# Kernel optimization log

Measured on AMD Instinct MI355X. Metric: run time of the kernel, lower is better.

The kernel has to match this reference:

```python
import jax, jax.numpy as jnp
import numpy as np

B, S, C, D, K = 8, 1024, 8192, 256, 512
FREEDOM = 0.1

def setup_inputs() -> dict:
    key = jax.random.key(0)
    k1, k2, k3 = jax.random.split(key, 3)
    concept_seq = jax.random.uniform(k1, (B, S, C), dtype=jnp.float32)
    concept_emb = jax.random.uniform(k2, (C, D), dtype=jnp.float32)  # nn.Parameter(torch.rand(max_c+1, d_model))
    centroid_emb = jax.random.uniform(k3, (K, D), dtype=jnp.float32)
    return {"concept_seq": concept_seq, "concept_emb": concept_emb,
            "centroid_emb": centroid_emb, "domain": 0}

def reference(concept_seq, concept_emb, centroid_emb, domain):
    # normalize multi-hot rows by their count (rows summing to 0 use count=1)
    cnt = jnp.sum(concept_seq, axis=-1, keepdims=True)
    cnt = jnp.where(cnt == 0, jnp.ones_like(cnt), cnt)
    cs = concept_seq / cnt
    # weighted embedding sum: [B,S,C] @ [C,D] -> [B,S,D]
    e_free = jnp.einsum('bsc,cd->bsd', cs, concept_emb)
    # nearest centroid (argmin of cdist == argmin of squared distance)
    flat = e_free.reshape(-1, D)                               # [B*S, D]
    d2 = (jnp.sum(flat * flat, axis=1, keepdims=True)
          - 2.0 * flat @ centroid_emb.T
          + jnp.sum(centroid_emb * centroid_emb, axis=1))      # [B*S, K]
    idx = jnp.argmin(d2, axis=1)                               # [B*S]
    e_cent = centroid_emb[idx].reshape(e_free.shape)           # [B,S,D]
    return e_free * FREEDOM + e_cent * (1.0 - FREEDOM)
```

## Files before the change

### kernel.cpp

```cpp
#include <hip/hip_runtime.h>


typedef unsigned short u16;
typedef unsigned int   u32;
using bf16x8 = __attribute__((ext_vector_type(8))) short;
using f32x4  = __attribute__((ext_vector_type(4))) float;
using f32x16 = __attribute__((ext_vector_type(16))) float;

#define MFMA_B16(A,B,C) __builtin_amdgcn_mfma_f32_16x16x32_bf16((A),(B),(C),0,0,0)
#define MFMA32(A,B,C)   __builtin_amdgcn_mfma_f32_32x32x16_bf16((A),(B),(C),0,0,0)

#define NSPLIT 4
#define SWZ(r) ((((r)&7) ^ (((r)>>3)&3)))

static __device__ __forceinline__ u16 f2bf(float f){
  u32 u = __builtin_bit_cast(u32, f);
  u += 0x7FFFu + ((u >> 16) & 1u);
  return (u16)(u >> 16);
}
static __device__ __forceinline__ u16 f2bf_fast(float f){
  u32 u = __builtin_bit_cast(u32, f);
  return (u16)((u + 0x8000u) >> 16);
}
static __device__ __forceinline__ float bf2f(u16 h){
  u32 u = ((u32)h) << 16;
  return __builtin_bit_cast(float, u);
}
static __device__ __forceinline__ void split2(float va, float vb, u32& hw, u32& lw){
  u16 ha = f2bf(va), hb = f2bf(vb);
  hw = (u32)ha | ((u32)hb << 16);
  lw = (u32)f2bf(va - bf2f(ha)) | ((u32)f2bf(vb - bf2f(hb)) << 16);
}
static __device__ __forceinline__ void split2f(float va, float vb, u32& hw, u32& lw){
  u16 ha = f2bf_fast(va), hb = f2bf_fast(vb);
  hw = (u32)ha | ((u32)hb << 16);
  lw = (u32)f2bf_fast(va - bf2f(ha)) | ((u32)f2bf_fast(vb - bf2f(hb)) << 16);
}

#define SZ_PART    ((size_t)NSPLIT*8192UL*256UL*4UL)
#define OFF_CNT    (SZ_PART)
#define SZ_CNT     ((size_t)NSPLIT*8192UL*4UL)
#define OFF_BHI    (OFF_CNT + SZ_CNT)
#define SZ_BHI     (8192UL*256UL*2UL)
#define OFF_BLO    (OFF_BHI + SZ_BHI)
#define OFF_CTHI   (OFF_BLO + SZ_BHI)
#define SZ_CT      (512UL*256UL*2UL)
#define OFF_CTLO   (OFF_CTHI + SZ_CT)
#define OFF_CNORM  (OFF_CTLO + SZ_CT)

__global__ __launch_bounds__(256) void ce_prep(
    const float* __restrict__ emb, const float* __restrict__ cent,
    u16* __restrict__ Bhi, u16* __restrict__ Blo,
    u16* __restrict__ CThi, u16* __restrict__ CTlo,
    double* __restrict__ cnormd)
{
  const int b = blockIdx.x, t = threadIdx.x;
  const int l = t & 63;
  if (b < 1024) {
    const int g  = b * 4 + (t >> 6);
    const int nt = g >> 9, ksg = g & 511;
    const int col = nt*32 + (l & 31);
    const int k0  = ksg*16 + (l >> 5)*8;
    u32 hw[4], lw[4];
    #pragma unroll
    for (int p = 0; p < 4; ++p) {
      float va = emb[(size_t)(k0 + 2*p    )*256 + col];
      float vb = emb[(size_t)(k0 + 2*p + 1)*256 + col];
      split2(va, vb, hw[p], lw[p]);
    }
    const size_t fi = ((size_t)nt*512 + ksg)*64 + l;
    *(uint4*)(Bhi + fi*8) = make_uint4(hw[0],hw[1],hw[2],hw[3]);
    *(uint4*)(Blo + fi*8) = make_uint4(lw[0],lw[1],lw[2],lw[3]);
  } else if (b < 1088) {
    const int lr = l & 15, lk = l >> 4;
    const int g  = (b - 1024) * 4 + (t >> 6);
    const int nt = g >> 3, ksg = g & 7;
    u32 hw[4], lw[4];
    #pragma unroll
    for (int p = 0; p < 4; ++p) {
      float va = cent[(size_t)(nt*16 + lr)*256 + ksg*32 + lk*8 + 2*p    ] - 0.5f;
      float vb = cent[(size_t)(nt*16 + lr)*256 + ksg*32 + lk*8 + 2*p + 1] - 0.5f;
      split2(va, vb, hw[p], lw[p]);
    }
    const size_t fi = ((size_t)nt*8 + ksg)*64 + l;
    *(uint4*)(CThi + fi*8) = make_uint4(hw[0],hw[1],hw[2],hw[3]);
    *(uint4*)(CTlo + fi*8) = make_uint4(lw[0],lw[1],lw[2],lw[3]);
  } else {
    const int row = (b - 1088)*8 + (t >> 5);
    const int h = t & 31;
    double s = 0.0;
    #pragma unroll
    for (int j = 0; j < 8; ++j) {
      float x = cent[(size_t)row*256 + h*8 + j] - 0.5f;
      s += (double)x * (double)x;
    }
    #pragma unroll
    for (int off = 16; off > 0; off >>= 1) s += __shfl_xor(s, off);
    if (h == 0) cnormd[row] = s;
  }
}

__global__ __launch_bounds__(512, 4) void ce_gemm(
    const float* __restrict__ seq,
    const u16* __restrict__ Bhi, const u16* __restrict__ Blo,
    float* __restrict__ part, float* __restrict__ cntpart)
{
  __shared__ char Ah[2][2*64*128];
  __shared__ char Al[2][2*64*128];

  const int t   = threadIdx.x;
  const int blk = blockIdx.x;
  const int mt  = blk >> 2;
  const int ks  = blk & 3;
  const size_t rowBase = (size_t)mt * 64;
  const int ar  = t >> 3;
  const int ac  = t & 7;
  const float* aptr = seq + (rowBase + ar) * 8192 + (size_t)ks * 2048 + ac * 16;

  const int w = t >> 6, l = t & 63;
  const int lrow = l & 31, lhi = l >> 5;

  f32x16 acc0 = {0.f}, acc1 = {0.f};
  #pragma unroll
  for (int i = 0; i < 16; ++i) { acc0[i] = 0.f; acc1[i] = 0.f; }

  float csum = 0.f;
  float4 areg[4];

  auto loadA = [&](void) {
    #pragma unroll
    for (int i = 0; i < 4; ++i) areg[i] = *(const float4*)(aptr + i*4);
  };
  auto stage8 = [&](int buf, int j) {
    const float4 A = areg[2*j], B = areg[2*j+1];
    float v[8] = {A.x, A.y, A.z, A.w, B.x, B.y, B.z, B.w};
    #pragma unroll
    for (int i = 0; i < 8; ++i) csum += v[i];
    u32 hw[4], lw[4];
    #pragma unroll
    for (int p = 0; p < 4; ++p) split2f(v[2*p], v[2*p+1], hw[p], lw[p]);
    const int slot = ((ac & 3) << 1) | j;
    const int off  = (ac >> 2)*8192 + ar*128 + ((slot ^ SWZ(ar)) << 4);
    *(uint4*)(Ah[buf] + off) = make_uint4(hw[0],hw[1],hw[2],hw[3]);
    *(uint4*)(Al[buf] + off) = make_uint4(lw[0],lw[1],lw[2],lw[3]);
  };

  bf16x8 bhA, blA, bhB, blB;
  auto loadB_A = [&](int ksg) {
    const size_t fi = (((size_t)w*512 + ksg)*64 + l)*8;
    bhA = *(const bf16x8*)(Bhi + fi);
    blA = *(const bf16x8*)(Blo + fi);
  };
  auto loadB_B = [&](int ksg) {
    const size_t fi = (((size_t)w*512 + ksg)*64 + l)*8;
    bhB = *(const bf16x8*)(Bhi + fi);
    blB = *(const bf16x8*)(Blo + fi);
  };
  auto cluster = [&](int buf, int ksub, bf16x8 bh, bf16x8 bl) {
    const int khalf = ksub >> 2;
    const int slot  = ((ksub & 3) << 1) | lhi;
    bf16x8 ah0, al0, ah1, al1;
    {
      const int r0 = lrow;
      const int o0 = khalf*8192 + r0*128 + ((slot ^ SWZ(r0)) << 4);
      ah0 = *(const bf16x8*)(Ah[buf] + o0);
      al0 = *(const bf16x8*)(Al[buf] + o0);
      const int r1 = 32 + lrow;
      const int o1 = khalf*8192 + r1*128 + ((slot ^ SWZ(r1)) << 4);
      ah1 = *(const bf16x8*)(Ah[buf] + o1);
      al1 = *(const bf16x8*)(Al[buf] + o1);
    }
    __builtin_amdgcn_s_setprio(1);
    acc0 = MFMA32(ah0, bh, acc0);
    acc1 = MFMA32(ah1, bh, acc1);
    acc0 = MFMA32(al0, bh, acc0);
    acc1 = MFMA32(al1, bh, acc1);
    acc0 = MFMA32(ah0, bl, acc0);
    acc1 = MFMA32(ah1, bl, acc1);
    __builtin_amdgcn_s_setprio(0);
  };

  loadA();
  stage8(0, 0);
  stage8(0, 1);
  aptr += 128;
  loadA();
  loadB_A(ks*128 + 0);
  __syncthreads();

  for (int step = 0; step < 16; ++step) {
    const int cur = step & 1;
    const int kb  = ks*128 + step*8;
    const bool more = (step < 15);

    loadB_B(kb + 1);
    if (more) stage8(cur^1, 0);
    cluster(cur, 0, bhA, blA);

    loadB_A(kb + 2);
    cluster(cur, 1, bhB, blB);

    loadB_B(kb + 3);
    if (more) stage8(cur^1, 1);
    cluster(cur, 2, bhA, blA);

    loadB_A(kb + 4);
    cluster(cur, 3, bhB, blB);

    loadB_B(kb + 5);
    if (step < 14) { aptr += 128; loadA(); }
    cluster(cur, 4, bhA, blA);

    loadB_A(kb + 6);
    cluster(cur, 5, bhB, blB);

    loadB_B(kb + 7);
    cluster(cur, 6, bhA, blA);

    if (more) loadB_A(kb + 8);
    cluster(cur, 7, bhB, blB);

    __syncthreads();
  }

  {
    float c = csum;
    c += __shfl_xor(c, 1);
    c += __shfl_xor(c, 2);
    c += __shfl_xor(c, 4);
    if (ac == 0) cntpart[(size_t)ks*8192 + rowBase + ar] = c;
  }
  float* pbase = part + ((size_t)ks*8192 + rowBase)*256;
  const int col = w*32 + lrow;
  #pragma unroll
  for (int reg = 0; reg < 16; ++reg) {
    const int rsub = (reg & 3) + 8*(reg >> 2) + 4*lhi;
    pbase[(size_t)(rsub     )*256 + col] = acc0[reg];
    pbase[(size_t)(rsub + 32)*256 + col] = acc1[reg];
  }
}

__global__ __launch_bounds__(256) void ce_cent(
    const float* __restrict__ part, const float* __restrict__ cntpart,
    const u16* __restrict__ CThi, const u16* __restrict__ CTlo,
    const double* __restrict__ cnormd, const float* __restrict__ cent,
    float* __restrict__ out)
{
  __shared__ float eL[32][256];
  __shared__ char Eh[32*512];
  __shared__ char El[32*512];
  __shared__ float GL[32][512];
  __shared__ float cntL[32];
  __shared__ float enred[32][8];
  __shared__ float enL[32];

  const int t = threadIdx.x;
  const size_t rb = (size_t)blockIdx.x * 32;
  const int r  = t >> 3;
  const int c0 = (t & 7) * 32;

  if (t < 32) {
    float s = 0.f;
    #pragma unroll
    for (int p = 0; p < NSPLIT; ++p) s += cntpart[(size_t)p*8192 + rb + t];
    cntL[t] = (s == 0.f) ? 1.f : s;
  }
  __syncthreads();
  const float inv = 1.0f / cntL[r];
  float en = 0.f;
  #pragma unroll
  for (int jp = 0; jp < 4; ++jp) {
    float e8[8];
    #pragma unroll
    for (int q = 0; q < 2; ++q) {
      const float* p0 = part + (rb + r)*256 + c0 + jp*8 + q*4;
      float4 e4 = {0.f, 0.f, 0.f, 0.f};
      #pragma unroll
      for (int p = 0; p < NSPLIT; ++p) {
        float4 s0 = *(const float4*)(p0 + (size_t)p*2097152);
        e4.x += s0.x; e4.y += s0.y; e4.z += s0.z; e4.w += s0.w;
      }
      e4.x *= inv; e4.y *= inv; e4.z *= inv; e4.w *= inv;
      *(float4*)&eL[r][c0 + jp*8 + q*4] = e4;
      e8[q*4+0] = e4.x; e8[q*4+1] = e4.y; e8[q*4+2] = e4.z; e8[q*4+3] = e4.w;
    }
    u32 hw[4], lw[4];
    #pragma unroll
    for (int p = 0; p < 4; ++p) {
      float va = e8[2*p] - 0.5f, vb = e8[2*p+1] - 0.5f;
      split2(va, vb, hw[p], lw[p]);
      en += va*va + vb*vb;
    }
    const int slot = (t & 7)*4 + jp;
    const int off  = r*512 + ((slot ^ (r & 7)) << 4);
    *(uint4*)(Eh + off) = make_uint4(hw[0],hw[1],hw[2],hw[3]);
    *(uint4*)(El + off) = make_uint4(lw[0],lw[1],lw[2],lw[3]);
  }
  enred[r][t & 7] = en;
  __syncthreads();
  if (t < 32) {
    float s = 0.f;
    #pragma unroll
    for (int j = 0; j < 8; ++j) s += enred[t][j];
    enL[t] = s;
  }
  const int w = t >> 6, l = t & 63, lr = l & 15, lk = l >> 4;
  f32x4 acc[2][8];
  #pragma unroll
  for (int i = 0; i < 2; ++i)
    #pragma unroll
    for (int j = 0; j < 8; ++j) acc[i][j] = (f32x4){0.f,0.f,0.f,0.f};
  #pragma unroll
  for (int ksub = 0; ksub < 8; ++ksub) {
    bf16x8 ah[2], alo[2];
    #pragma unroll
    for (int mi = 0; mi < 2; ++mi) {
      const int row = mi*16 + lr;
      const int off = row*512 + (((ksub*4 + lk) ^ (row & 7)) << 4);
      ah[mi]  = *(const bf16x8*)(Eh + off);
      alo[mi] = *(const bf16x8*)(El + off);
    }
    bf16x8 bh[8], bl[8];
    #pragma unroll
    for (int ni = 0; ni < 8; ++ni) {
      const size_t fi = (((size_t)(w*8 + ni))*8 + ksub)*64 + l;
      bh[ni] = *(const bf16x8*)(CThi + fi*8);
      bl[ni] = *(const bf16x8*)(CTlo + fi*8);
    }
    #pragma unroll
    for (int mi = 0; mi < 2; ++mi)
      #pragma unroll
      for (int ni = 0; ni < 8; ++ni) {
        acc[mi][ni] = MFMA_B16(ah[mi],  bh[ni], acc[mi][ni]);
        acc[mi][ni] = MFMA_B16(alo[mi], bh[ni], acc[mi][ni]);
        acc[mi][ni] = MFMA_B16(ah[mi],  bl[ni], acc[mi][ni]);
      }
  }
  #pragma unroll
  for (int mi = 0; mi < 2; ++mi)
    #pragma unroll
    for (int ni = 0; ni < 8; ++ni)
      #pragma unroll
      for (int rr = 0; rr < 4; ++rr)
        GL[mi*16 + lk*4 + rr][w*128 + ni*16 + lr] = acc[mi][ni][rr];
  __syncthreads();
  for (int i = 0; i < 8; ++i) {
    const int row = w*8 + i;
    const double en_ = (double)enL[row];
    double best = 1e300; int bk = 0;
    #pragma unroll
    for (int jj = 0; jj < 8; ++jj) {
      const int k = jj*64 + l;
      const double d2 = en_ + cnormd[k] - 2.0*(double)GL[row][k];
      if (d2 < best) { best = d2; bk = k; }
    }
    #pragma unroll
    for (int off = 32; off > 0; off >>= 1) {
      const double ov = __shfl_xor(best, off);
      const int   ok = __shfl_xor(bk, off);
      if (ov < best || (ov == best && ok < bk)) { best = ov; bk = ok; }
    }
    const float* crow = cent + (size_t)bk*256;
    float4 ef = *(const float4*)&eL[row][l*4];
    float4 cf = *(const float4*)(crow + l*4);
    float4 o;
    o.x = 0.1f*ef.x + 0.9f*cf.x;
    o.y = 0.1f*ef.y + 0.9f*cf.y;
    o.z = 0.1f*ef.z + 0.9f*cf.z;
    o.w = 0.1f*ef.w + 0.9f*cf.w;
    *(float4*)(out + (rb + row)*256 + l*4) = o;
  }
}

extern "C" void kernel_launch(void* const* d_in, const int* in_sizes, int n_in,
                              void* d_out, int out_size, void* d_ws, size_t ws_size,
                              hipStream_t stream) {
  const float* seq  = (const float*)d_in[0];
  const float* emb  = (const float*)d_in[1];
  const float* cent = (const float*)d_in[2];
  float* out = (float*)d_out;
  char* ws = (char*)d_ws;

  float*  part    = (float*) (ws);
  float*  cntpart = (float*) (ws + OFF_CNT);
  u16*    Bhi     = (u16*)   (ws + OFF_BHI);
  u16*    Blo     = (u16*)   (ws + OFF_BLO);
  u16*    CThi    = (u16*)   (ws + OFF_CTHI);
  u16*    CTlo    = (u16*)   (ws + OFF_CTLO);
  double* cnormd  = (double*)(ws + OFF_CNORM);

  hipLaunchKernelGGL(ce_prep, dim3(1152), dim3(256), 0, stream,
                     emb, cent, Bhi, Blo, CThi, CTlo, cnormd);
  hipLaunchKernelGGL(ce_gemm, dim3(512), dim3(512), 0, stream,
                     seq, Bhi, Blo, part, cntpart);
  hipLaunchKernelGGL(ce_cent, dim3(256), dim3(256), 0, stream,
                     part, cntpart, CThi, CTlo, cnormd, cent, out);
}
```

Before: 143.4 us.

## Load A operand directly into registers per wave, drop LDS staging

The GEMM kernel no longer stages the split bf16 A tile through double-buffered shared memory with barriers. Each wave now loads its own fp32 A fragments straight from global memory in MFMA layout, splits them to hi/lo bf16 in registers, and feeds the MFMAs. This removes LDS traffic and __syncthreads, but each of the 8 waves in a block reloads the same A rows and redoes the split, an eightfold increase in global/L2 reads and conversion ALU work. The row-count sum is now computed only by wave 0.

```diff
diff --git a/kernel.cpp b/kernel.cpp
--- a/kernel.cpp
+++ b/kernel.cpp
@@ -11,7 +11,6 @@
 #define MFMA32(A,B,C)   __builtin_amdgcn_mfma_f32_32x32x16_bf16((A),(B),(C),0,0,0)
 
 #define NSPLIT 4
-#define SWZ(r) ((((r)&7) ^ (((r)>>3)&3)))
 
 static __device__ __forceinline__ u16 f2bf(float f){
   u32 u = __builtin_bit_cast(u32, f);
@@ -105,131 +104,104 @@
     const u16* __restrict__ Bhi, const u16* __restrict__ Blo,
     float* __restrict__ part, float* __restrict__ cntpart)
 {
-  __shared__ char Ah[2][2*64*128];
-  __shared__ char Al[2][2*64*128];
-
   const int t   = threadIdx.x;
   const int blk = blockIdx.x;
   const int mt  = blk >> 2;
   const int ks  = blk & 3;
   const size_t rowBase = (size_t)mt * 64;
-  const int ar  = t >> 3;
-  const int ac  = t & 7;
-  const float* aptr = seq + (rowBase + ar) * 8192 + (size_t)ks * 2048 + ac * 16;
 
   const int w = t >> 6, l = t & 63;
   const int lrow = l & 31, lhi = l >> 5;
-
-  f32x16 acc0 = {0.f}, acc1 = {0.f};
+  const int kx = lhi * 8;
+
+  const float* a0 = seq + (rowBase + lrow) * 8192 + (size_t)ks * 2048 + kx;
+  const float* a1 = a0 + (size_t)32 * 8192;
+  const size_t bbase = ((size_t)w * 512 + (size_t)ks * 128) * 64 * 8 + (size_t)l * 8;
+
+  f32x16 acc0, acc1;
   #pragma unroll
   for (int i = 0; i < 16; ++i) { acc0[i] = 0.f; acc1[i] = 0.f; }
 
-  float csum = 0.f;
-  float4 areg[4];
-
-  auto loadA = [&](void) {
-    #pragma unroll
-    for (int i = 0; i < 4; ++i) areg[i] = *(const float4*)(aptr + i*4);
+  float c0 = 0.f, c1 = 0.f;
+  const bool doC = (w == 0);
+
+  auto split8 = [&](float4 x, float4 y, bf16x8& ah, bf16x8& al, float& cs) {
+    float v[8] = {x.x, x.y, x.z, x.w, y.x, y.y, y.z, y.w};
+    if (doC) {
+      #pragma unroll
+      for (int i = 0; i < 8; ++i) cs += v[i];
+    }
+    u32 hw[4], lw[4];
+    #pragma unroll
+    for (int p = 0; p < 4; ++p) split2f(v[2*p], v[2*p+1], hw[p], lw[p]);
+    ah = __builtin_bit_cast(bf16x8, make_uint4(hw[0],hw[1],hw[2],hw[3]));
+    al = __builtin_bit_cast(bf16x8, make_uint4(lw[0],lw[1],lw[2],lw[3]));
   };
-  auto stage8 = [&](int buf, int j) {
-    const float4 A = areg[2*j], B = areg[2*j+1];
-    float v[8] = {A.x, A.y, A.z, A.w, B.x, B.y, B.z, B.w};
-    #pragma unroll
-    for (int i = 0; i < 8; ++i) csum += v[i];
-    u32 hw[4], lw[4];
-    #pragma unroll
-    for (int p = 0; p < 4; ++p) split2f(v[2*p], v[2*p+1], hw[p], lw[p]);
-    const int slot = ((ac & 3) << 1) | j;
-    const int off  = (ac >> 2)*8192 + ar*128 + ((slot ^ SWZ(ar)) << 4);
-    *(uint4*)(Ah[buf] + off) = make_uint4(hw[0],hw[1],hw[2],hw[3]);
-    *(uint4*)(Al[buf] + off) = make_uint4(lw[0],lw[1],lw[2],lw[3]);
-  };
-
+
+  float4 fA0, fA1, fA2, fA3;
+  float4 fB0, fB1, fB2, fB3;
   bf16x8 bhA, blA, bhB, blB;
-  auto loadB_A = [&](int ksg) {
-    const size_t fi = (((size_t)w*512 + ksg)*64 + l)*8;
-    bhA = *(const bf16x8*)(Bhi + fi);
-    blA = *(const bf16x8*)(Blo + fi);
-  };
-  auto loadB_B = [&](int ksg) {
-    const size_t fi = (((size_t)w*512 + ksg)*64 + l)*8;
-    bhB = *(const bf16x8*)(Bhi + fi);
-    blB = *(const bf16x8*)(Blo + fi);
-  };
-  auto cluster = [&](int buf, int ksub, bf16x8 bh, bf16x8 bl) {
-    const int khalf = ksub >> 2;
-    const int slot  = ((ksub & 3) << 1) | lhi;
-    bf16x8 ah0, al0, ah1, al1;
+
+  fA0 = *(const float4*)(a0);     fA1 = *(const float4*)(a0 + 4);
+  fA2 = *(const float4*)(a1);     fA3 = *(const float4*)(a1 + 4);
+  bhA = *(const bf16x8*)(Bhi + bbase);
+  blA = *(const bf16x8*)(Blo + bbase);
+
+  for (int s = 0; s < 128; s += 2) {
     {
-      const int r0 = lrow;
-      const int o0 = khalf*8192 + r0*128 + ((slot ^ SWZ(r0)) << 4);
-      ah0 = *(const bf16x8*)(Ah[buf] + o0);
-      al0 = *(const bf16x8*)(Al[buf] + o0);
-      const int r1 = 32 + lrow;
-      const int o1 = khalf*8192 + r1*128 + ((slot ^ SWZ(r1)) << 4);
-      ah1 = *(const bf16x8*)(Ah[buf] + o1);
-      al1 = *(const bf16x8*)(Al[buf] + o1);
-    }
-    __builtin_amdgcn_s_setprio(1);
-    acc0 = MFMA32(ah0, bh, acc0);
-    acc1 = MFMA32(ah1, bh, acc1);
-    acc0 = MFMA32(al0, bh, acc0);
-    acc1 = MFMA32(al1, bh, acc1);
-    acc0 = MFMA32(ah0, bl, acc0);
-    acc1 = MFMA32(ah1, bl, acc1);
-    __builtin_amdgcn_s_setprio(0);
-  };
-
-  loadA();
-  stage8(0, 0);
-  stage8(0, 1);
-  aptr += 128;
-  loadA();
-  loadB_A(ks*128 + 0);
-  __syncthreads();
-
-  for (int step = 0; step < 16; ++step) {
-    const int cur = step & 1;
-    const int kb  = ks*128 + step*8;
-    const bool more = (step < 15);
-
-    loadB_B(kb + 1);
-    if (more) stage8(cur^1, 0);
-    cluster(cur, 0, bhA, blA);
-
-    loadB_A(kb + 2);
-    cluster(cur, 1, bhB, blB);
-
-    loadB_B(kb + 3);
-    if (more) stage8(cur^1, 1);
-    cluster(cur, 2, bhA, blA);
-
-    loadB_A(kb + 4);
-    cluster(cur, 3, bhB, blB);
-
-    loadB_B(kb + 5);
-    if (step < 14) { aptr += 128; loadA(); }
-    cluster(cur, 4, bhA, blA);
-
-    loadB_A(kb + 6);
-    cluster(cur, 5, bhB, blB);
-
-    loadB_B(kb + 7);
-    cluster(cur, 6, bhA, blA);
-
-    if (more) loadB_A(kb + 8);
-    cluster(cur, 7, bhB, blB);
-
-    __syncthreads();
-  }
-
-  {
-    float c = csum;
-    c += __shfl_xor(c, 1);
-    c += __shfl_xor(c, 2);
-    c += __shfl_xor(c, 4);
-    if (ac == 0) cntpart[(size_t)ks*8192 + rowBase + ar] = c;
-  }
+      const size_t ao = (size_t)(s + 1) * 16;
+      fB0 = *(const float4*)(a0 + ao);     fB1 = *(const float4*)(a0 + ao + 4);
+      fB2 = *(const float4*)(a1 + ao);     fB3 = *(const float4*)(a1 + ao + 4);
+      const size_t bo = bbase + (size_t)(s + 1) * 512;
+      bhB = *(const bf16x8*)(Bhi + bo);
+      blB = *(const bf16x8*)(Blo + bo);
+    }
+    {
+      bf16x8 ah0, al0, ah1, al1;
+      split8(fA0, fA1, ah0, al0, c0);
+      split8(fA2, fA3, ah1, al1, c1);
+      __builtin_amdgcn_s_setprio(1);
+      acc0 = MFMA32(ah0, bhA, acc0);
+      acc1 = MFMA32(ah1, bhA, acc1);
+      acc0 = MFMA32(al0, bhA, acc0);
+      acc1 = MFMA32(al1, bhA, acc1);
+      acc0 = MFMA32(ah0, blA, acc0);
+      acc1 = MFMA32(ah1, blA, acc1);
+      __builtin_amdgcn_s_setprio(0);
+    }
+    {
+      const int ns = (s + 2 < 128) ? (s + 2) : 127;
+      const size_t ao = (size_t)ns * 16;
+      fA0 = *(const float4*)(a0 + ao);     fA1 = *(const float4*)(a0 + ao + 4);
+      fA2 = *(const float4*)(a1 + ao);     fA3 = *(const float4*)(a1 + ao + 4);
+      const size_t bo = bbase + (size_t)ns * 512;
+      bhA = *(const bf16x8*)(Bhi + bo);
+      blA = *(const bf16x8*)(Blo + bo);
+    }
+    {
+      bf16x8 ah0, al0, ah1, al1;
+      split8(fB0, fB1, ah0, al0, c0);
+      split8(fB2, fB3, ah1, al1, c1);
+      __builtin_amdgcn_s_setprio(1);
+      acc0 = MFMA32(ah0, bhB, acc0);
+      acc1 = MFMA32(ah1, bhB, acc1);
+      acc0 = MFMA32(al0, bhB, acc0);
+      acc1 = MFMA32(al1, bhB, acc1);
+      acc0 = MFMA32(ah0, blB, acc0);
+      acc1 = MFMA32(ah1, blB, acc1);
+      __builtin_amdgcn_s_setprio(0);
+    }
+  }
+
+  if (doC) {
+    c0 += __shfl_xor(c0, 32);
+    c1 += __shfl_xor(c1, 32);
+    if (l < 32) {
+      cntpart[(size_t)ks*8192 + rowBase + l]      = c0;
+      cntpart[(size_t)ks*8192 + rowBase + 32 + l] = c1;
+    }
+  }
+
   float* pbase = part + ((size_t)ks*8192 + rowBase)*256;
   const int col = w*32 + lrow;
   #pragma unroll
```

Result: slower. 331.1 us (+131.0%).

## Retile concept GEMM to 128-row blocks with 2x2 warp tiles and 8-way K split

Applied to the files above, without the earlier changes.

The first GEMM now works on 128-row M tiles with an 8-way K split of 1024 each, where it previously used 64-row tiles with a 4-way split. Each wave computes a 64x64 output tile (a 2x2 grid of 32x32 MFMAs) instead of 64x32. This improves reuse of the bf16 hi/lo B fragments and A tiles loaded from LDS, and halves the B fragment traffic per output row. In exchange it doubles accumulator registers, which may reduce occupancy under launch_bounds(512,4). It also doubles the partial-sum buffer the downstream reduction must read, and the LDS swizzle changes to a simple XOR.

```diff
diff --git a/kernel.cpp b/kernel.cpp
--- a/kernel.cpp
+++ b/kernel.cpp
@@ -10,8 +10,7 @@
 #define MFMA_B16(A,B,C) __builtin_amdgcn_mfma_f32_16x16x32_bf16((A),(B),(C),0,0,0)
 #define MFMA32(A,B,C)   __builtin_amdgcn_mfma_f32_32x32x16_bf16((A),(B),(C),0,0,0)
 
-#define NSPLIT 4
-#define SWZ(r) ((((r)&7) ^ (((r)>>3)&3)))
+#define NSPLIT 8
 
 static __device__ __forceinline__ u16 f2bf(float f){
   u32 u = __builtin_bit_cast(u32, f);
@@ -105,24 +104,25 @@
     const u16* __restrict__ Bhi, const u16* __restrict__ Blo,
     float* __restrict__ part, float* __restrict__ cntpart)
 {
-  __shared__ char Ah[2][2*64*128];
-  __shared__ char Al[2][2*64*128];
+  __shared__ char Ah[2][128*128];
+  __shared__ char Al[2][128*128];
 
   const int t   = threadIdx.x;
   const int blk = blockIdx.x;
-  const int mt  = blk >> 2;
-  const int ks  = blk & 3;
-  const size_t rowBase = (size_t)mt * 64;
-  const int ar  = t >> 3;
-  const int ac  = t & 7;
-  const float* aptr = seq + (rowBase + ar) * 8192 + (size_t)ks * 2048 + ac * 16;
+  const int mt  = blk >> 3;
+  const int ks  = blk & 7;
+  const size_t rowBase = (size_t)mt * 128;
+  const int ar  = t >> 2;
+  const int ac  = t & 3;
+  const float* aptr = seq + (rowBase + ar) * 8192 + (size_t)ks * 1024 + ac * 16;
 
   const int w = t >> 6, l = t & 63;
+  const int wm = w >> 2, wn = w & 3;
   const int lrow = l & 31, lhi = l >> 5;
 
-  f32x16 acc0 = {0.f}, acc1 = {0.f};
-  #pragma unroll
-  for (int i = 0; i < 16; ++i) { acc0[i] = 0.f; acc1[i] = 0.f; }
+  f32x16 acc00, acc01, acc10, acc11;
+  #pragma unroll
+  for (int i = 0; i < 16; ++i) { acc00[i]=0.f; acc01[i]=0.f; acc10[i]=0.f; acc11[i]=0.f; }
 
   float csum = 0.f;
   float4 areg[4];
@@ -139,86 +139,78 @@
     u32 hw[4], lw[4];
     #pragma unroll
     for (int p = 0; p < 4; ++p) split2f(v[2*p], v[2*p+1], hw[p], lw[p]);
-    const int slot = ((ac & 3) << 1) | j;
-    const int off  = (ac >> 2)*8192 + ar*128 + ((slot ^ SWZ(ar)) << 4);
+    const int slot = ac*2 + j;
+    const int off  = ar*128 + ((slot ^ (ar & 7)) << 4);
     *(uint4*)(Ah[buf] + off) = make_uint4(hw[0],hw[1],hw[2],hw[3]);
     *(uint4*)(Al[buf] + off) = make_uint4(lw[0],lw[1],lw[2],lw[3]);
   };
 
-  bf16x8 bhA, blA, bhB, blB;
+  bf16x8 bhA0, blA0, bhA1, blA1, bhB0, blB0, bhB1, blB1;
   auto loadB_A = [&](int ksg) {
-    const size_t fi = (((size_t)w*512 + ksg)*64 + l)*8;
-    bhA = *(const bf16x8*)(Bhi + fi);
-    blA = *(const bf16x8*)(Blo + fi);
+    const size_t f0 = (((size_t)(wn*2    ))*512 + ksg)*64*8 + (size_t)l*8;
+    const size_t f1 = (((size_t)(wn*2 + 1))*512 + ksg)*64*8 + (size_t)l*8;
+    bhA0 = *(const bf16x8*)(Bhi + f0);  blA0 = *(const bf16x8*)(Blo + f0);
+    bhA1 = *(const bf16x8*)(Bhi + f1);  blA1 = *(const bf16x8*)(Blo + f1);
   };
   auto loadB_B = [&](int ksg) {
-    const size_t fi = (((size_t)w*512 + ksg)*64 + l)*8;
-    bhB = *(const bf16x8*)(Bhi + fi);
-    blB = *(const bf16x8*)(Blo + fi);
-  };
-  auto cluster = [&](int buf, int ksub, bf16x8 bh, bf16x8 bl) {
-    const int khalf = ksub >> 2;
-    const int slot  = ((ksub & 3) << 1) | lhi;
-    bf16x8 ah0, al0, ah1, al1;
-    {
-      const int r0 = lrow;
-      const int o0 = khalf*8192 + r0*128 + ((slot ^ SWZ(r0)) << 4);
-      ah0 = *(const bf16x8*)(Ah[buf] + o0);
-      al0 = *(const bf16x8*)(Al[buf] + o0);
-      const int r1 = 32 + lrow;
-      const int o1 = khalf*8192 + r1*128 + ((slot ^ SWZ(r1)) << 4);
-      ah1 = *(const bf16x8*)(Ah[buf] + o1);
-      al1 = *(const bf16x8*)(Al[buf] + o1);
-    }
+    const size_t f0 = (((size_t)(wn*2    ))*512 + ksg)*64*8 + (size_t)l*8;
+    const size_t f1 = (((size_t)(wn*2 + 1))*512 + ksg)*64*8 + (size_t)l*8;
+    bhB0 = *(const bf16x8*)(Bhi + f0);  blB0 = *(const bf16x8*)(Blo + f0);
+    bhB1 = *(const bf16x8*)(Bhi + f1);  blB1 = *(const bf16x8*)(Blo + f1);
+  };
+  auto cluster = [&](int buf, int ksub, bf16x8 bh0, bf16x8 bl0, bf16x8 bh1, bf16x8 bl1) {
+    const int slot = ksub*2 + lhi;
+    const int r0 = wm*64 + lrow;
+    const int r1 = r0 + 32;
+    const int o0 = r0*128 + ((slot ^ (r0 & 7)) << 4);
+    const int o1 = r1*128 + ((slot ^ (r1 & 7)) << 4);
+    bf16x8 ah0 = *(const bf16x8*)(Ah[buf] + o0);
+    bf16x8 al0 = *(const bf16x8*)(Al[buf] + o0);
+    bf16x8 ah1 = *(const bf16x8*)(Ah[buf] + o1);
+    bf16x8 al1 = *(const bf16x8*)(Al[buf] + o1);
     __builtin_amdgcn_s_setprio(1);
-    acc0 = MFMA32(ah0, bh, acc0);
-    acc1 = MFMA32(ah1, bh, acc1);
-    acc0 = MFMA32(al0, bh, acc0);
-    acc1 = MFMA32(al1, bh, acc1);
-    acc0 = MFMA32(ah0, bl, acc0);
-    acc1 = MFMA32(ah1, bl, acc1);
+    acc00 = MFMA32(ah0, bh0, acc00);
+    acc01 = MFMA32(ah0, bh1, acc01);
+    acc10 = MFMA32(ah1, bh0, acc10);
+    acc11 = MFMA32(ah1, bh1, acc11);
+    acc00 = MFMA32(al0, bh0, acc00);
+    acc01 = MFMA32(al0, bh1, acc01);
+    acc10 = MFMA32(al1, bh0, acc10);
+    acc11 = MFMA32(al1, bh1, acc11);
+    acc00 = MFMA32(ah0, bl0, acc00);
+    acc01 = MFMA32(ah0, bl1, acc01);
+    acc10 = MFMA32(ah1, bl0, acc10);
+    acc11 = MFMA32(ah1, bl1, acc11);
     __builtin_amdgcn_s_setprio(0);
   };
 
   loadA();
   stage8(0, 0);
   stage8(0, 1);
-  aptr += 128;
+  aptr += 64;
   loadA();
-  loadB_A(ks*128 + 0);
+  loadB_A(ks*64 + 0);
   __syncthreads();
 
   for (int step = 0; step < 16; ++step) {
     const int cur = step & 1;
-    const int kb  = ks*128 + step*8;
+    const int kb  = ks*64 + step*4;
     const bool more = (step < 15);
 
     loadB_B(kb + 1);
     if (more) stage8(cur^1, 0);
-    cluster(cur, 0, bhA, blA);
+    cluster(cur, 0, bhA0, blA0, bhA1, blA1);
 
     loadB_A(kb + 2);
-    cluster(cur, 1, bhB, blB);
+    if (more) stage8(cur^1, 1);
+    cluster(cur, 1, bhB0, blB0, bhB1, blB1);
 
     loadB_B(kb + 3);
-    if (more) stage8(cur^1, 1);
-    cluster(cur, 2, bhA, blA);
-
-    loadB_A(kb + 4);
-    cluster(cur, 3, bhB, blB);
-
-    loadB_B(kb + 5);
-    if (step < 14) { aptr += 128; loadA(); }
-    cluster(cur, 4, bhA, blA);
-
-    loadB_A(kb + 6);
-    cluster(cur, 5, bhB, blB);
-
-    loadB_B(kb + 7);
-    cluster(cur, 6, bhA, blA);
-
-    if (more) loadB_A(kb + 8);
-    cluster(cur, 7, bhB, blB);
+    if (step < 14) { aptr += 64; loadA(); }
+    cluster(cur, 2, bhA0, blA0, bhA1, blA1);
+
+    if (more) loadB_A(kb + 4);
+    cluster(cur, 3, bhB0, blB0, bhB1, blB1);
 
     __syncthreads();
   }
@@ -227,16 +219,18 @@
     float c = csum;
     c += __shfl_xor(c, 1);
     c += __shfl_xor(c, 2);
-    c += __shfl_xor(c, 4);
-    if (ac == 0) cntpart[(size_t)ks*8192 + rowBase + ar] = c;
+    if ((l & 3) == 0) cntpart[(size_t)ks*8192 + rowBase + ar] = c;
   }
   float* pbase = part + ((size_t)ks*8192 + rowBase)*256;
-  const int col = w*32 + lrow;
+  const int c0 = wn*64 + lrow;
   #pragma unroll
   for (int reg = 0; reg < 16; ++reg) {
     const int rsub = (reg & 3) + 8*(reg >> 2) + 4*lhi;
-    pbase[(size_t)(rsub     )*256 + col] = acc0[reg];
-    pbase[(size_t)(rsub + 32)*256 + col] = acc1[reg];
+    const int r0 = wm*64 + rsub;
+    pbase[(size_t)(r0     )*256 + c0     ] = acc00[reg];
+    pbase[(size_t)(r0     )*256 + c0 + 32] = acc01[reg];
+    pbase[(size_t)(r0 + 32)*256 + c0     ] = acc10[reg];
+    pbase[(size_t)(r0 + 32)*256 + c0 + 32] = acc11[reg];
   }
 }
 
```

Measured after the change: 285.0 us. 1.99x slower.
